# Performance work log

Hardware: AMD Instinct MI355X
Metric: run time of the kernel (lower is better)

Reference implementation:

```python
import jax, jax.numpy as jnp
import numpy as np

N_FFT = 64
HOP = 8
PATCH = 100
N_FRAMES = (PATCH - N_FFT) // HOP + 1   # 5
N_FREQ = N_FFT // 2 + 1                 # 33


def _hann_periodic(n):
    # torch.hann_window(n) is periodic: 0.5*(1 - cos(2*pi*k/n))
    k = jnp.arange(n, dtype=jnp.float32)
    return 0.5 * (1.0 - jnp.cos(2.0 * jnp.pi * k / n))


def setup_inputs() -> dict:
    key = jax.random.key(0)
    patches = jax.random.normal(key, (128, 2048, PATCH), dtype=jnp.float32)
    return {"patches": patches}


def reference(patches) -> jnp.ndarray:
    # patches: (B, N, P) or (M, P); math identical, fully vectorized.
    window = _hann_periodic(N_FFT)
    # frame index matrix: (n_frames, n_fft)
    idx = jnp.arange(N_FRAMES)[:, None] * HOP + jnp.arange(N_FFT)[None, :]
    frames = patches[..., idx] * window                 # (..., n_frames, n_fft)
    spec = jnp.fft.rfft(frames, axis=-1)                # (..., n_frames, n_freq)
    log_mag = jnp.log1p(jnp.abs(spec))
    # torch.stft layout is (..., freq, frames); flatten in that order -> freq-major
    log_mag = jnp.swapaxes(log_mag, -1, -2)             # (..., n_freq, n_frames)
    out_shape = patches.shape[:-1] + (N_FREQ * N_FRAMES,)
    return log_mag.reshape(out_shape)                   # (..., 165)
```

## Files before the change

kernel.cpp:

```cpp
#include <hip/hip_runtime.h>
#include <math.h>


#define ROWS_PER_BLOCK 64
#define BLOCK_THREADS (ROWS_PER_BLOCK * 5)
#define ROW_LEN 100
#define OUT_PER_ROW 165

constexpr float W32C[16] = {
    1.0f, 0.980785280403230f, 0.923879532511287f, 0.831469612302545f,
    0.707106781186548f, 0.555570233019602f, 0.382683432365090f, 0.195090322016128f,
    0.0f, -0.195090322016128f, -0.382683432365090f, -0.555570233019602f,
    -0.707106781186548f, -0.831469612302545f, -0.923879532511287f, -0.980785280403230f};
constexpr float W32S[16] = {
    0.0f, 0.195090322016128f, 0.382683432365090f, 0.555570233019602f,
    0.707106781186548f, 0.831469612302545f, 0.923879532511287f, 0.980785280403230f,
    1.0f, 0.980785280403230f, 0.923879532511287f, 0.831469612302545f,
    0.707106781186548f, 0.555570233019602f, 0.382683432365090f, 0.195090322016128f};

constexpr float TC[33] = {
    1.0f, 0.995184726672197f, 0.980785280403230f, 0.956940335732209f,
    0.923879532511287f, 0.881921264348355f, 0.831469612302545f, 0.773010453362737f,
    0.707106781186548f, 0.634393284163645f, 0.555570233019602f, 0.471396736825998f,
    0.382683432365090f, 0.290284677254462f, 0.195090322016128f, 0.098017140329561f,
    0.0f, -0.098017140329561f, -0.195090322016128f, -0.290284677254462f,
    -0.382683432365090f, -0.471396736825998f, -0.555570233019602f, -0.634393284163645f,
    -0.707106781186548f, -0.773010453362737f, -0.831469612302545f, -0.881921264348355f,
    -0.923879532511287f, -0.956940335732209f, -0.980785280403230f, -0.995184726672197f,
    -1.0f};
constexpr float TS[33] = {
    0.0f, 0.098017140329561f, 0.195090322016128f, 0.290284677254462f,
    0.382683432365090f, 0.471396736825998f, 0.555570233019602f, 0.634393284163645f,
    0.707106781186548f, 0.773010453362737f, 0.831469612302545f, 0.881921264348355f,
    0.923879532511287f, 0.956940335732209f, 0.980785280403230f, 0.995184726672197f,
    1.0f, 0.995184726672197f, 0.980785280403230f, 0.956940335732209f,
    0.923879532511287f, 0.881921264348355f, 0.831469612302545f, 0.773010453362737f,
    0.707106781186548f, 0.634393284163645f, 0.555570233019602f, 0.471396736825998f,
    0.382683432365090f, 0.290284677254462f, 0.195090322016128f, 0.098017140329561f};

constexpr int BR32[32] = {0, 16, 8, 24, 4, 20, 12, 28, 2, 18, 10, 26, 6, 22, 14, 30,
                          1, 17, 9, 25, 5, 21, 13, 29, 3, 19, 11, 27, 7, 23, 15, 31};

__device__ __forceinline__ constexpr float hann_half(int n) {
    return 0.25f * (1.0f - TC[(n <= 32) ? n : (64 - n)]);
}

__global__ __launch_bounds__(BLOCK_THREADS, 2)
void SpectralTokenizer_36103495090536_kernel(const float* __restrict__ in,
                                             float* __restrict__ out,
                                             int nrows) {
    __shared__ float so[ROWS_PER_BLOCK * OUT_PER_ROW];

    const int tid = threadIdx.x;
    const int row_local = tid / 5;
    const int frame = tid - row_local * 5;
    const long long row = (long long)blockIdx.x * ROWS_PER_BLOCK + row_local;
    const bool active = (row < (long long)nrows);

    float ar[32], ai[32];

    if (active) {
        const float4* src = (const float4*)(in + row * ROW_LEN + frame * 8);
#pragma unroll
        for (int i = 0; i < 16; i++) {
            float4 v = src[i];
            const int p0 = BR32[2 * i], p1 = BR32[2 * i + 1];
            ar[p0] = v.x * hann_half(4 * i + 0);
            ai[p0] = v.y * hann_half(4 * i + 1);
            ar[p1] = v.z * hann_half(4 * i + 2);
            ai[p1] = v.w * hann_half(4 * i + 3);
        }

#define BUTTERFLY(i0, i1, c, sn)                                   \
        {                                                          \
            float tr = (c) * ar[i1] + (sn) * ai[i1];               \
            float ti = (c) * ai[i1] - (sn) * ar[i1];               \
            float ur = ar[i0], ui = ai[i0];                        \
            ar[i0] = ur + tr; ai[i0] = ui + ti;                    \
            ar[i1] = ur - tr; ai[i1] = ui - ti;                    \
        }

#pragma unroll
        for (int t = 0; t < 16; t++) BUTTERFLY(2 * t, 2 * t + 1, 1.0f, 0.0f);
#pragma unroll
        for (int t = 0; t < 8; t++) {
            const int k = 4 * t;
            BUTTERFLY(k + 0, k + 2, 1.0f, 0.0f);
            BUTTERFLY(k + 1, k + 3, 0.0f, 1.0f);
        }
#pragma unroll
        for (int t = 0; t < 4; t++) {
            const int k = 8 * t;
            BUTTERFLY(k + 0, k + 4, 1.0f, 0.0f);
            BUTTERFLY(k + 1, k + 5, W32C[4], W32S[4]);
            BUTTERFLY(k + 2, k + 6, 0.0f, 1.0f);
            BUTTERFLY(k + 3, k + 7, W32C[12], W32S[12]);
        }
#pragma unroll
        for (int t = 0; t < 2; t++) {
            const int k = 16 * t;
#pragma unroll
            for (int j = 0; j < 8; j++) BUTTERFLY(k + j, k + j + 8, W32C[2 * j], W32S[2 * j]);
        }
#pragma unroll
        for (int j = 0; j < 16; j++) BUTTERFLY(j, j + 16, W32C[j], W32S[j]);
#undef BUTTERFLY

        float* orow = so + row_local * OUT_PER_ROW + frame;
#pragma unroll
        for (int k = 0; k <= 32; k++) {
            const int km = k & 31;
            const int kc = (32 - k) & 31;
            const float er = ar[km] + ar[kc];
            const float ei = ai[km] - ai[kc];
            const float pr = ai[km] + ai[kc];
            const float pi = ar[kc] - ar[km];
            const float xr = er + TC[k] * pr + TS[k] * pi;
            const float xi = ei + TC[k] * pi - TS[k] * pr;
            const float mag = sqrtf(xr * xr + xi * xi);
            orow[k * 5] = __logf(1.0f + mag);
        }
    }

    __syncthreads();

    const long long block_base = (long long)blockIdx.x * (ROWS_PER_BLOCK * OUT_PER_ROW);
    const long long total_out = (long long)nrows * OUT_PER_ROW;
    float4* dst = (float4*)(out + block_base);
    const float4* s4 = (const float4*)so;
#pragma unroll 2
    for (int t = tid; t < (ROWS_PER_BLOCK * OUT_PER_ROW / 4); t += BLOCK_THREADS) {
        if (block_base + 4 * t + 3 < total_out) dst[t] = s4[t];
    }
}

extern "C" void kernel_launch(void* const* d_in, const int* in_sizes, int n_in,
                              void* d_out, int out_size, void* d_ws, size_t ws_size,
                              hipStream_t stream) {
    const float* in = (const float*)d_in[0];
    float* out = (float*)d_out;
    const int nrows = in_sizes[0] / ROW_LEN;
    const int grid = (nrows + ROWS_PER_BLOCK - 1) / ROWS_PER_BLOCK;
    hipLaunchKernelGGL(SpectralTokenizer_36103495090536_kernel,
                       dim3(grid), dim3(BLOCK_THREADS), 0, stream, in, out, nrows);
}
```

Measured before the change: 266.7 us.

## Split each 32-point FFT across two lanes with shuffle-based final stage

Each frame's 32-point complex FFT is now split between a pair of adjacent threads, each computing a 16-point FFT on half the bit-reversed inputs. The last butterfly stage and the real-FFT post-processing use cross-lane shuffles. Block size doubles and the occupancy hint rises, to cut per-thread register pressure and expose more parallelism. The cost is extra shuffle instructions, redundant twiddle math with selects, and narrower float2 loads. Fast hardware sqrt is also used for the magnitude.

Result: slower. 302.1 us (+13.3%).

```diff
diff --git a/kernel.cpp b/kernel.cpp
--- a/kernel.cpp
+++ b/kernel.cpp
@@ -3,7 +3,7 @@
 
 
 #define ROWS_PER_BLOCK 64
-#define BLOCK_THREADS (ROWS_PER_BLOCK * 5)
+#define BLOCK_THREADS (ROWS_PER_BLOCK * 5 * 2)
 #define ROW_LEN 100
 #define OUT_PER_ROW 165
 
@@ -38,37 +38,38 @@
     0.707106781186548f, 0.634393284163645f, 0.555570233019602f, 0.471396736825998f,
     0.382683432365090f, 0.290284677254462f, 0.195090322016128f, 0.098017140329561f};
 
-constexpr int BR32[32] = {0, 16, 8, 24, 4, 20, 12, 28, 2, 18, 10, 26, 6, 22, 14, 30,
-                          1, 17, 9, 25, 5, 21, 13, 29, 3, 19, 11, 27, 7, 23, 15, 31};
+constexpr int BR16[16] = {0, 8, 4, 12, 2, 10, 6, 14, 1, 9, 5, 13, 3, 11, 7, 15};
 
 __device__ __forceinline__ constexpr float hann_half(int n) {
     return 0.25f * (1.0f - TC[(n <= 32) ? n : (64 - n)]);
 }
 
-__global__ __launch_bounds__(BLOCK_THREADS, 2)
+__global__ __launch_bounds__(BLOCK_THREADS, 4)
 void SpectralTokenizer_36103495090536_kernel(const float* __restrict__ in,
                                              float* __restrict__ out,
                                              int nrows) {
     __shared__ float so[ROWS_PER_BLOCK * OUT_PER_ROW];
 
     const int tid = threadIdx.x;
-    const int row_local = tid / 5;
-    const int frame = tid - row_local * 5;
+    const int h = tid & 1;
+    const int pair = tid >> 1;
+    const int row_local = pair / 5;
+    const int frame = pair - row_local * 5;
     const long long row = (long long)blockIdx.x * ROWS_PER_BLOCK + row_local;
     const bool active = (row < (long long)nrows);
 
-    float ar[32], ai[32];
+    float ar[16], ai[16];
 
     if (active) {
-        const float4* src = (const float4*)(in + row * ROW_LEN + frame * 8);
+        const float2* src = (const float2*)(in + row * ROW_LEN + frame * 8);
 #pragma unroll
-        for (int i = 0; i < 16; i++) {
-            float4 v = src[i];
-            const int p0 = BR32[2 * i], p1 = BR32[2 * i + 1];
-            ar[p0] = v.x * hann_half(4 * i + 0);
-            ai[p0] = v.y * hann_half(4 * i + 1);
-            ar[p1] = v.z * hann_half(4 * i + 2);
-            ai[p1] = v.w * hann_half(4 * i + 3);
+        for (int q = 0; q < 16; q++) {
+            const int m = BR16[q];
+            float2 v = src[2 * m + h];
+            const float wa = h ? hann_half(4 * m + 2) : hann_half(4 * m + 0);
+            const float wb = h ? hann_half(4 * m + 3) : hann_half(4 * m + 1);
+            ar[q] = v.x * wa;
+            ai[q] = v.y * wb;
         }
 
 #define BUTTERFLY(i0, i1, c, sn)                                   \
@@ -81,15 +82,15 @@
         }
 
 #pragma unroll
-        for (int t = 0; t < 16; t++) BUTTERFLY(2 * t, 2 * t + 1, 1.0f, 0.0f);
+        for (int t = 0; t < 8; t++) BUTTERFLY(2 * t, 2 * t + 1, 1.0f, 0.0f);
 #pragma unroll
-        for (int t = 0; t < 8; t++) {
+        for (int t = 0; t < 4; t++) {
             const int k = 4 * t;
             BUTTERFLY(k + 0, k + 2, 1.0f, 0.0f);
             BUTTERFLY(k + 1, k + 3, 0.0f, 1.0f);
         }
 #pragma unroll
-        for (int t = 0; t < 4; t++) {
+        for (int t = 0; t < 2; t++) {
             const int k = 8 * t;
             BUTTERFLY(k + 0, k + 4, 1.0f, 0.0f);
             BUTTERFLY(k + 1, k + 5, W32C[4], W32S[4]);
@@ -97,28 +98,50 @@
             BUTTERFLY(k + 3, k + 7, W32C[12], W32S[12]);
         }
 #pragma unroll
-        for (int t = 0; t < 2; t++) {
-            const int k = 16 * t;
-#pragma unroll
-            for (int j = 0; j < 8; j++) BUTTERFLY(k + j, k + j + 8, W32C[2 * j], W32S[2 * j]);
-        }
-#pragma unroll
-        for (int j = 0; j < 16; j++) BUTTERFLY(j, j + 16, W32C[j], W32S[j]);
+        for (int j = 0; j < 8; j++) BUTTERFLY(j, j + 8, W32C[2 * j], W32S[2 * j]);
 #undef BUTTERFLY
 
+#pragma unroll
+        for (int q = 0; q < 16; q++) {
+            const float c = W32C[q], s = W32S[q];
+            const float twr = c * ar[q] + s * ai[q];
+            const float twi = c * ai[q] - s * ar[q];
+            const float sr = h ? twr : ar[q];
+            const float si = h ? twi : ai[q];
+            const float rr = __shfl_xor(sr, 1);
+            const float ri = __shfl_xor(si, 1);
+            ar[q] = h ? (rr - twr) : (ar[q] + rr);
+            ai[q] = h ? (ri - twi) : (ai[q] + ri);
+        }
+
         float* orow = so + row_local * OUT_PER_ROW + frame;
+        float* orow2 = orow + 80 * h;
+
+        {
+            const float a0r = ar[0], a0i = ai[0];
+            const float v0 = __logf(1.0f + fabsf(2.0f * (a0r + a0i)));
+            const float v16 = __logf(1.0f + 2.0f * __builtin_amdgcn_sqrtf(
+                                  fmaf(a0r, a0r, a0i * a0i)));
+            orow2[0] = h ? v16 : v0;
+            if (!h) orow[160] = __logf(1.0f + fabsf(2.0f * (a0r - a0i)));
+        }
+
 #pragma unroll
-        for (int k = 0; k <= 32; k++) {
-            const int km = k & 31;
-            const int kc = (32 - k) & 31;
-            const float er = ar[km] + ar[kc];
-            const float ei = ai[km] - ai[kc];
-            const float pr = ai[km] + ai[kc];
-            const float pi = ar[kc] - ar[km];
-            const float xr = er + TC[k] * pr + TS[k] * pi;
-            const float xi = ei + TC[k] * pi - TS[k] * pr;
-            const float mag = sqrtf(xr * xr + xi * xi);
-            orow[k * 5] = __logf(1.0f + mag);
+        for (int k = 1; k < 16; k++) {
+            const float rr = __shfl_xor(ar[16 - k], 1);
+            const float ri = __shfl_xor(ai[16 - k], 1);
+            const float er = ar[k] + rr;
+            const float ei = ai[k] - ri;
+            const float pr = ai[k] + ri;
+            const float pi = rr - ar[k];
+            const float npr = -pr;
+            const float C = TC[k], S = TS[k];
+            const float A1 = h ? pi : pr, B1 = h ? npr : pi;
+            const float A2 = h ? npr : pi, B2 = h ? pi : pr;
+            const float xr = er + C * A1 + S * B1;
+            const float xi = ei + C * A2 - S * B2;
+            const float mag = __builtin_amdgcn_sqrtf(fmaf(xr, xr, xi * xi));
+            orow2[k * 5] = __logf(1.0f + mag);
         }
     }
 
@@ -128,7 +151,6 @@
     const long long total_out = (long long)nrows * OUT_PER_ROW;
     float4* dst = (float4*)(out + block_base);
     const float4* s4 = (const float4*)so;
-#pragma unroll 2
     for (int t = tid; t < (ROWS_PER_BLOCK * OUT_PER_ROW / 4); t += BLOCK_THREADS) {
         if (block_base + 4 * t + 3 < total_out) dst[t] = s4[t];
     }
```
